# Optimization experiments

Measured on AMD Instinct MI355X. Metric: run time of the kernel, lower is better.

Reference implementation:

```python
import jax, jax.numpy as jnp
import numpy as np

D_K = 512  # attn_dim

def setup_inputs() -> dict:
    key = jax.random.key(0)
    ks = jax.random.split(key, 10)
    B, S, D, A, Dv = 8, 2048, 1024, 512, 512
    Q = jax.random.normal(ks[0], (B, S, D), dtype=jnp.float32)
    K = jax.random.normal(ks[1], (B, S, D), dtype=jnp.float32)
    V = jax.random.normal(ks[2], (B, S, D), dtype=jnp.float32)
    attn_mask = jax.random.randint(ks[3], (B, S, S), 0, 2, dtype=jnp.int32)
    s = 1.0 / np.sqrt(D)
    Wq = jax.random.normal(ks[4], (A, D), dtype=jnp.float32) * s
    bq = jnp.zeros((A,), dtype=jnp.float32)
    Wk = jax.random.normal(ks[5], (A, D), dtype=jnp.float32) * s
    bk = jnp.zeros((A,), dtype=jnp.float32)
    Wv = jax.random.normal(ks[6], (Dv, D), dtype=jnp.float32) * s
    bv = jnp.zeros((Dv,), dtype=jnp.float32)
    return {"Q": Q, "K": K, "V": V, "attn_mask": attn_mask,
            "Wq": Wq, "bq": bq, "Wk": Wk, "bk": bk, "Wv": Wv, "bv": bv}

def reference(Q, K, V, attn_mask, Wq, bq, Wk, bk, Wv, bv):
    # Linear projections (torch Linear: x @ W.T + b)
    Qp = jnp.einsum('bsd,ad->bsa', Q, Wq) + bq          # [B,S,A]
    Kp = jnp.einsum('bsd,ad->bsa', K, Wk) + bk          # [B,S,A]
    WV = jnp.einsum('bsd,vd->bsv', V, Wv) + bv          # [B,S,Dv]
    scale = 1.0 / np.sqrt(D_K).astype(np.float32)
    scores = jnp.einsum('bqa,bka->bqk', Qp, Kp) * scale  # [B,S,S]
    scores = scores + attn_mask.astype(scores.dtype) * (-1e9)
    scores = jnp.swapaxes(scores, -1, -2)               # transpose BEFORE softmax
    attn = jax.nn.softmax(scores, axis=-1)              # normalize over query axis
    selfOutput = jnp.einsum('bkq,bqv->bkv', attn, WV)   # [B,S,Dv]
    return selfOutput, attn
```

## Files before the change

### kernel.cpp

```cpp
#include <hip/hip_runtime.h>
#include <stdint.h>

#define B_N   8
#define S_N   2048
#define D_N   1024
#define A_N   512
#define DV_N  512

typedef __attribute__((ext_vector_type(8))) short bf16x8;
typedef __attribute__((ext_vector_type(4))) float f32x4;

__device__ __forceinline__ unsigned short f2bf(float x) {
    union { float f; unsigned int u; } v; v.f = x;
    return (unsigned short)((v.u + 0x7fffu + ((v.u >> 16) & 1u)) >> 16);
}
__device__ __forceinline__ float bf2f(unsigned short h) {
    union { unsigned int u; float f; } v; v.u = ((unsigned int)h) << 16;
    return v.f;
}

__global__ void cvt3_f32_bf16(const float* __restrict__ s0, const float* __restrict__ s1,
                              const float* __restrict__ s2,
                              unsigned short* __restrict__ d0, unsigned short* __restrict__ d1,
                              unsigned short* __restrict__ d2, int n4) {
    const float* s = (blockIdx.z == 0) ? s0 : (blockIdx.z == 1) ? s1 : s2;
    unsigned short* d = (blockIdx.z == 0) ? d0 : (blockIdx.z == 1) ? d1 : d2;
    int i = blockIdx.x * blockDim.x + threadIdx.x;
    if (i >= n4) return;
    float4 v = ((const float4*)s)[i];
    ushort4 o;
    o.x = f2bf(v.x); o.y = f2bf(v.y); o.z = f2bf(v.z); o.w = f2bf(v.w);
    ((ushort4*)d)[i] = o;
}

__global__ void zero_f32(float* __restrict__ p, int n) {
    int i = blockIdx.x * blockDim.x + threadIdx.x;
    if (i < n) p[i] = 0.0f;
}

__device__ __forceinline__ void gld_lds16(const void* g, void* l) {
    __builtin_amdgcn_global_load_lds(
        (const __attribute__((address_space(1))) unsigned int*)g,
        (__attribute__((address_space(3))) unsigned int*)l, 16, 0, 0);
}

__global__ __launch_bounds__(256) void pack_maskT(const int* __restrict__ mask,
                                                  unsigned int* __restrict__ mpT) {
    __shared__ int tile[64 * 129];
    const int b  = blockIdx.z;
    const int q0 = blockIdx.y * 64;
    const int k0 = blockIdx.x * 128;
    const int tid = threadIdx.x;
    const long long base = (long long)b * S_N * S_N;
#pragma unroll
    for (int it = 0; it < 8; ++it) {
        int c = it * 256 + tid;
        int row  = c >> 5;
        int col4 = (c & 31) * 4;
        int4 v = *(const int4*)&mask[base + (long long)(q0 + row) * S_N + k0 + col4];
        int* d = &tile[row * 129 + col4];
        d[0] = v.x; d[1] = v.y; d[2] = v.z; d[3] = v.w;
    }
    __syncthreads();
    const int wave = tid >> 6, lane = tid & 63;
#pragma unroll
    for (int kk = 0; kk < 32; ++kk) {
        const int k = wave * 32 + kk;
        const int v = tile[lane * 129 + k];
        const unsigned long long bal = __ballot(v != 0);
        if (lane == 0) {
            unsigned int* o = &mpT[(long long)(b * S_N + k0 + k) * 64 + (q0 >> 5)];
            o[0] = (unsigned int)bal;
            o[1] = (unsigned int)(bal >> 32);
        }
    }
}

template <int MODE>
__global__ __launch_bounds__(256) void gemm_nt(
    const unsigned short* __restrict__ A, const unsigned short* __restrict__ B,
    const unsigned short* __restrict__ B2,
    void* __restrict__ C, const float* __restrict__ bias, const float* __restrict__ bias2,
    const unsigned int* __restrict__ mpT, float* __restrict__ rowsum,
    int M, int N, int K,
    long long sA, long long sB, long long sC, float scale)
{
    __shared__ __align__(16) unsigned short As[128 * 32];
    __shared__ __align__(16) unsigned short Bs[128 * 32];

    const int tid  = threadIdx.x;
    const int wave = tid >> 6;
    const int lane = tid & 63;
    const int lrow = lane & 15;
    const int quad = lane >> 4;
    const int wm = wave & 1;
    const int wn = wave >> 1;
    const int b  = blockIdx.z;
    const int m0 = blockIdx.y * 128;
    const int n0 = blockIdx.x * 128;

    const unsigned short* Ab = A + (long long)b * sA;
    const unsigned short* Bsel = (MODE == 0 && blockIdx.y >= 128) ? B2 : B;
    const unsigned short* Bb = Bsel + (long long)b * sB;
    const float* bias_s = (MODE == 0 && blockIdx.y >= 128) ? bias2 : bias;

    f32x4 acc[4][4];
#pragma unroll
    for (int i = 0; i < 4; ++i)
#pragma unroll
        for (int j = 0; j < 4; ++j) acc[i][j] = (f32x4){0.f, 0.f, 0.f, 0.f};

    const int srow = lane >> 2;
    const int scol = (lane & 3) * 8;

    for (int kt = 0; kt < K; kt += 32) {
#pragma unroll
        for (int t = 0; t < 2; ++t) {
            const int seg = t * 4 + wave;
            const unsigned short* ga =
                Ab + (long long)(m0 + seg * 16 + srow) * K + kt + scol;
            gld_lds16(ga, &As[seg * 16 * 32]);
            const unsigned short* gb =
                Bb + (long long)(n0 + seg * 16 + srow) * K + kt + scol;
            gld_lds16(gb, &Bs[seg * 16 * 32]);
        }
        __syncthreads();

        bf16x8 af[4], bfr[4];
#pragma unroll
        for (int i = 0; i < 4; ++i)
            af[i] = *(const bf16x8*)&As[(wm * 64 + i * 16 + lrow) * 32 + quad * 8];
#pragma unroll
        for (int j = 0; j < 4; ++j)
            bfr[j] = *(const bf16x8*)&Bs[(wn * 64 + j * 16 + lrow) * 32 + quad * 8];
#pragma unroll
        for (int i = 0; i < 4; ++i)
#pragma unroll
            for (int j = 0; j < 4; ++j)
                acc[i][j] = __builtin_amdgcn_mfma_f32_16x16x32_bf16(
                    af[i], bfr[j], acc[i][j], 0, 0, 0);
        __syncthreads();
    }

    if (MODE == 0 || MODE == 1) {
#pragma unroll
        for (int i = 0; i < 4; ++i) {
            const int rowb = m0 + wm * 64 + i * 16 + quad * 4;
#pragma unroll
            for (int j = 0; j < 4; ++j) {
                const int col = n0 + wn * 64 + j * 16 + lrow;
#pragma unroll
                for (int r = 0; r < 4; ++r) {
                    const int row = rowb + r;
                    float v = acc[i][j][r];
                    v += (MODE == 0) ? bias_s[col] : bias_s[row];
                    (((unsigned short*)C) + (long long)b * sC)
                        [(long long)row * N + col] = f2bf(v);
                }
            }
        }
    } else if (MODE == 2) {
        unsigned short* Cb = ((unsigned short*)C) + (long long)b * sC;
        const unsigned int* mpb = mpT + ((long long)b * S_N) * 64;
        float* rs = rowsum + (long long)b * S_N;
#pragma unroll
        for (int i = 0; i < 4; ++i) {
#pragma unroll
            for (int r = 0; r < 4; ++r) {
                const int row = m0 + wm * 64 + i * 16 + quad * 4 + r;
                const unsigned int* mpr = mpb + (long long)row * 64;
                float rsum = 0.0f;
#pragma unroll
                for (int j = 0; j < 4; ++j) {
                    const int col = n0 + wn * 64 + j * 16 + lrow;
                    const float v = acc[i][j][r] * scale;
                    const unsigned int w = mpr[col >> 5];
                    const float e = ((w >> (col & 31)) & 1u) ? 0.0f : __expf(v);
                    const unsigned short h = f2bf(e);
                    Cb[(long long)row * S_N + col] = h;
                    rsum += bf2f(h);
                }
                rsum += __shfl_xor(rsum, 1);
                rsum += __shfl_xor(rsum, 2);
                rsum += __shfl_xor(rsum, 4);
                rsum += __shfl_xor(rsum, 8);
                if (lrow == 0) atomicAdd(&rs[row], rsum);
            }
        }
    } else {
        float* Cb = ((float*)C) + (long long)b * sC;
        const float* rs = rowsum + (long long)b * S_N;
#pragma unroll
        for (int i = 0; i < 4; ++i) {
#pragma unroll
            for (int r = 0; r < 4; ++r) {
                const int row = m0 + wm * 64 + i * 16 + quad * 4 + r;
                const float inv = 1.0f / rs[row];
#pragma unroll
                for (int j = 0; j < 4; ++j) {
                    const int col = n0 + wn * 64 + j * 16 + lrow;
                    Cb[(long long)row * N + col] = acc[i][j][r] * inv;
                }
            }
        }
    }
}

__global__ __launch_bounds__(256) void normalize_rows(
    const unsigned short* __restrict__ ebf, const float* __restrict__ rowsum,
    float* __restrict__ attn)
{
    const long long row = blockIdx.x;
    const float inv = 1.0f / rowsum[row];
    const ushort4* src = (const ushort4*)(ebf + row * S_N);
    float4* dst = (float4*)(attn + row * S_N);
    const int tid = threadIdx.x;
#pragma unroll
    for (int t = 0; t < 2; ++t) {
        ushort4 h = src[tid + t * 256];
        float4 o;
        o.x = bf2f(h.x) * inv;
        o.y = bf2f(h.y) * inv;
        o.z = bf2f(h.z) * inv;
        o.w = bf2f(h.w) * inv;
        dst[tid + t * 256] = o;
    }
}

extern "C" void kernel_launch(void* const* d_in, const int* in_sizes, int n_in,
                              void* d_out, int out_size, void* d_ws, size_t ws_size,
                              hipStream_t stream) {
    const float* Q    = (const float*)d_in[0];
    const float* K    = (const float*)d_in[1];
    const float* V    = (const float*)d_in[2];
    const int*   mask = (const int*)d_in[3];
    const float* Wq   = (const float*)d_in[4];
    const float* bq   = (const float*)d_in[5];
    const float* Wk   = (const float*)d_in[6];
    const float* bk   = (const float*)d_in[7];
    const float* Wv   = (const float*)d_in[8];
    const float* bv   = (const float*)d_in[9];

    float* out      = (float*)d_out;
    float* attn_out = out + (long long)B_N * S_N * DV_N;

    unsigned short* Qbf  = (unsigned short*)d_ws;
    unsigned short* Kbf  = Qbf + (long long)B_N * S_N * D_N;
    unsigned short* attn_bf = Qbf;
    unsigned short* Vbf  = Kbf + (long long)B_N * S_N * D_N;
    unsigned short* Wqbf = Vbf + (long long)B_N * S_N * D_N;
    unsigned short* Wkbf = Wqbf + (long long)A_N * D_N;
    unsigned short* Wvbf = Wkbf + (long long)A_N * D_N;
    unsigned short* Qp   = Wvbf + (long long)DV_N * D_N;
    unsigned short* Kp   = Qp + (long long)B_N * S_N * A_N;
    unsigned short* WVt  = Kp + (long long)B_N * S_N * A_N;
    unsigned int*   mpT  = (unsigned int*)(WVt + (long long)B_N * DV_N * S_N);
    float*          rowsum = (float*)(mpT + (long long)B_N * S_N * 64);

    const float scale = 0.044194173824159216f;

    zero_f32<<<dim3((B_N * S_N) / 256), dim3(256), 0, stream>>>(rowsum, B_N * S_N);
    pack_maskT<<<dim3(S_N / 128, S_N / 64, B_N), dim3(256), 0, stream>>>(mask, mpT);

    {
        int n4 = (int)((long long)B_N * S_N * D_N / 4);
        cvt3_f32_bf16<<<dim3((n4 + 255) / 256, 1, 3), dim3(256), 0, stream>>>(
            Q, K, V, Qbf, Kbf, Vbf, n4);
        int w4 = (int)((long long)A_N * D_N / 4);
        cvt3_f32_bf16<<<dim3((w4 + 255) / 256, 1, 3), dim3(256), 0, stream>>>(
            Wq, Wk, Wv, Wqbf, Wkbf, Wvbf, w4);
    }

    gemm_nt<0><<<dim3(A_N / 128, (2 * B_N * S_N) / 128, 1), dim3(256), 0, stream>>>(
        Qbf, Wqbf, Wkbf, (void*)Qp, bq, bk, nullptr, nullptr,
        2 * B_N * S_N, A_N, D_N, 0, 0, 0, 1.0f);
    gemm_nt<1><<<dim3(S_N / 128, DV_N / 128, B_N), dim3(256), 0, stream>>>(
        Wvbf, Vbf, nullptr, (void*)WVt, bv, nullptr, nullptr, nullptr,
        DV_N, S_N, D_N, 0, (long long)S_N * D_N, (long long)DV_N * S_N, 1.0f);
    gemm_nt<2><<<dim3(S_N / 128, S_N / 128, B_N), dim3(256), 0, stream>>>(
        Kp, Qp, nullptr, (void*)attn_bf, nullptr, nullptr, mpT, rowsum,
        S_N, S_N, A_N, (long long)S_N * A_N, (long long)S_N * A_N,
        (long long)S_N * S_N, scale);
    normalize_rows<<<dim3(B_N * S_N), dim3(256), 0, stream>>>(attn_bf, rowsum, attn_out);
    gemm_nt<3><<<dim3(DV_N / 128, S_N / 128, B_N), dim3(256), 0, stream>>>(
        attn_bf, WVt, nullptr, (void*)out, nullptr, nullptr, nullptr, rowsum,
        S_N, DV_N, S_N, (long long)S_N * S_N, (long long)DV_N * S_N,
        (long long)S_N * DV_N, 1.0f);
}
```

Baseline: 678.0 us.

## Add 256x256-tile 8-wave pipelined GEMM for projection and score kernels

Introduces gemm_nt8, a 512-thread kernel with 256x256 output tiles and a double-buffered 128KB LDS. Global-to-LDS loads are interleaved with MFMA phases under explicit vmcnt waits and setprio, and it replaces the 128x128 GEMM for the Q/K projection and the masked score/exp stage. The aim is more data reuse per tile and overlap of loads with matrix math. In exchange it raises register and LDS pressure, which cuts occupancy, and its hand-tuned waitcnt sequencing is fragile.

```diff
diff --git a/kernel.cpp b/kernel.cpp
--- a/kernel.cpp
+++ b/kernel.cpp
@@ -206,6 +206,171 @@
     }
 }
 
+#define VMCNT(n) asm volatile("s_waitcnt vmcnt(" #n ")" ::: "memory")
+
+template <int MODE>
+__global__ __launch_bounds__(512, 2) void gemm_nt8(
+    const unsigned short* __restrict__ A, const unsigned short* __restrict__ B,
+    const unsigned short* __restrict__ B2,
+    void* __restrict__ C, const float* __restrict__ bias, const float* __restrict__ bias2,
+    const unsigned int* __restrict__ mpT, float* __restrict__ rowsum,
+    int M, int N, int K,
+    long long sA, long long sB, long long sC, float scale)
+{
+    extern __shared__ unsigned short sm[];
+
+    const int tid  = threadIdx.x;
+    const int w    = tid >> 6;
+    const int lane = tid & 63;
+    const int lrow = lane & 15;
+    const int quad = lane >> 4;
+    const int wmSel = w >> 2;
+    const int wn    = w & 3;
+    const int bhSel = wn >> 1;
+    const int b  = blockIdx.z;
+    const int m0 = blockIdx.y * 256;
+    const int n0 = blockIdx.x * 256;
+
+    const unsigned short* Ab = A + (long long)b * sA;
+    const unsigned short* Bsel = (MODE == 0 && blockIdx.y >= 64) ? B2 : B;
+    const unsigned short* Bb = Bsel + (long long)b * sB;
+    const float* bias_s = (MODE == 0 && blockIdx.y >= 64) ? bias2 : bias;
+
+    const int csw0 = ((quad ^ (lrow & 7)) << 4);
+    const int csw1 = csw0 ^ 64;
+    const int cswSt = (((lane & 7) ^ (lane >> 3)) << 3);
+
+    const unsigned short* srcA =
+        Ab + (size_t)(m0 + (w >> 2) * 128 + (w & 3) * 16 + (lane >> 3)) * K + cswSt;
+    const unsigned short* srcB =
+        Bb + (size_t)(n0 + (w >> 2) * 128 + ((w >> 1) & 1) * 64 + (w & 1) * 16 + (lane >> 3)) * K + cswSt;
+
+#define STAGE_A(par, mq, tk) do {                                              \
+        const unsigned short* s_ = srcA + (size_t)(mq) * 64 * K + (size_t)(tk) * 64; \
+        unsigned short* d_ = &sm[(par) * 16384 + (w >> 2) * 8192 +             \
+                                 ((mq) * 64 + (w & 3) * 16) * 64];             \
+        gld_lds16(s_, d_);                                                     \
+        gld_lds16(s_ + 8 * (size_t)K, d_ + 8 * 64);                            \
+    } while (0)
+
+#define STAGE_B(par, nq, tk) do {                                              \
+        const unsigned short* s_ = srcB + (size_t)(nq) * 32 * K + (size_t)(tk) * 64; \
+        unsigned short* d_ = &sm[32768 + (par) * 16384 + (w >> 2) * 8192 +     \
+                                 (((w >> 1) & 1) * 64 + (nq) * 32 + (w & 1) * 16) * 64]; \
+        gld_lds16(s_, d_);                                                     \
+        gld_lds16(s_ + 8 * (size_t)K, d_ + 8 * 64);                            \
+    } while (0)
+
+    f32x4 acc[8][4];
+#pragma unroll
+    for (int i = 0; i < 8; ++i)
+#pragma unroll
+        for (int j = 0; j < 4; ++j) acc[i][j] = (f32x4){0.f, 0.f, 0.f, 0.f};
+
+#define PHASE(par, mq, nq, STAGE_STMT, WAIT_STMT) do {                         \
+        bf16x8 af[4][2], bfr[2][2];                                            \
+        const int abase_ = (par) * 16384 + wmSel * 8192 + (mq) * 4096;         \
+        _Pragma("unroll")                                                      \
+        for (int m_ = 0; m_ < 4; ++m_) {                                       \
+            af[m_][0] = *(const bf16x8*)&sm[abase_ + (m_ * 16 + lrow) * 64 + (csw0 >> 1)]; \
+            af[m_][1] = *(const bf16x8*)&sm[abase_ + (m_ * 16 + lrow) * 64 + (csw1 >> 1)]; \
+        }                                                                      \
+        const int bbase_ = 32768 + (par) * 16384 + bhSel * 8192 +              \
+                           ((wn & 1) * 64 + (nq) * 32) * 64;                   \
+        _Pragma("unroll")                                                      \
+        for (int n_ = 0; n_ < 2; ++n_) {                                       \
+            bfr[n_][0] = *(const bf16x8*)&sm[bbase_ + (n_ * 16 + lrow) * 64 + (csw0 >> 1)]; \
+            bfr[n_][1] = *(const bf16x8*)&sm[bbase_ + (n_ * 16 + lrow) * 64 + (csw1 >> 1)]; \
+        }                                                                      \
+        STAGE_STMT;                                                            \
+        WAIT_STMT;                                                             \
+        __builtin_amdgcn_s_barrier();                                          \
+        __builtin_amdgcn_s_setprio(1);                                         \
+        _Pragma("unroll")                                                      \
+        for (int m_ = 0; m_ < 4; ++m_)                                         \
+            _Pragma("unroll")                                                  \
+            for (int n_ = 0; n_ < 2; ++n_) {                                   \
+                acc[(mq)*4+m_][(nq)*2+n_] = __builtin_amdgcn_mfma_f32_16x16x32_bf16( \
+                    af[m_][0], bfr[n_][0], acc[(mq)*4+m_][(nq)*2+n_], 0, 0, 0); \
+                acc[(mq)*4+m_][(nq)*2+n_] = __builtin_amdgcn_mfma_f32_16x16x32_bf16( \
+                    af[m_][1], bfr[n_][1], acc[(mq)*4+m_][(nq)*2+n_], 0, 0, 0); \
+            }                                                                  \
+        __builtin_amdgcn_s_setprio(0);                                         \
+        __builtin_amdgcn_s_barrier();                                          \
+    } while (0)
+
+    const int NT = K >> 6;
+
+    STAGE_A(0, 0, 0); STAGE_B(0, 0, 0);
+    STAGE_A(0, 1, 0); STAGE_B(0, 1, 0);
+    STAGE_A(1, 0, 1); STAGE_B(1, 0, 1);
+    VMCNT(8);
+    __builtin_amdgcn_s_barrier();
+
+    for (int t = 0; t < NT; t += 2) {
+        const int t2 = (t + 2 < NT) ? t + 2 : NT - 1;
+        const int t3 = (t + 3 < NT) ? t + 3 : NT - 1;
+        PHASE(0, 0, 0, STAGE_A(1, 1, t + 1), VMCNT(6));
+        PHASE(0, 0, 1, STAGE_B(1, 1, t + 1), VMCNT(10));
+        PHASE(0, 1, 0, STAGE_A(0, 0, t2),    (void)0);
+        PHASE(0, 1, 1, STAGE_B(0, 0, t2),    VMCNT(8));
+        PHASE(1, 0, 0, STAGE_A(0, 1, t2),    VMCNT(6));
+        PHASE(1, 0, 1, STAGE_B(0, 1, t2),    VMCNT(10));
+        PHASE(1, 1, 0, STAGE_A(1, 0, t3),    (void)0);
+        PHASE(1, 1, 1, STAGE_B(1, 0, t3),    VMCNT(8));
+    }
+    VMCNT(0);
+
+    if (MODE == 0) {
+#pragma unroll
+        for (int i = 0; i < 8; ++i) {
+            const int rowb = m0 + wmSel * 128 + i * 16 + quad * 4;
+#pragma unroll
+            for (int j = 0; j < 4; ++j) {
+                const int col = n0 + wn * 64 + j * 16 + lrow;
+#pragma unroll
+                for (int r = 0; r < 4; ++r) {
+                    const int row = rowb + r;
+                    float v = acc[i][j][r] + bias_s[col];
+                    (((unsigned short*)C) + (long long)b * sC)
+                        [(long long)row * N + col] = f2bf(v);
+                }
+            }
+        }
+    } else {
+        unsigned short* Cb = ((unsigned short*)C) + (long long)b * sC;
+        const unsigned int* mpb = mpT + ((long long)b * S_N) * 64;
+        float* rs = rowsum + (long long)b * S_N;
+#pragma unroll
+        for (int i = 0; i < 8; ++i) {
+#pragma unroll
+            for (int r = 0; r < 4; ++r) {
+                const int row = m0 + wmSel * 128 + i * 16 + quad * 4 + r;
+                const unsigned int* mpr = mpb + (long long)row * 64;
+                float rsum = 0.0f;
+#pragma unroll
+                for (int j = 0; j < 4; ++j) {
+                    const int col = n0 + wn * 64 + j * 16 + lrow;
+                    const float v = acc[i][j][r] * scale;
+                    const unsigned int wbits = mpr[col >> 5];
+                    const float e = ((wbits >> (col & 31)) & 1u) ? 0.0f : __expf(v);
+                    const unsigned short h = f2bf(e);
+                    Cb[(long long)row * S_N + col] = h;
+                    rsum += bf2f(h);
+                }
+                rsum += __shfl_xor(rsum, 1);
+                rsum += __shfl_xor(rsum, 2);
+                rsum += __shfl_xor(rsum, 4);
+                rsum += __shfl_xor(rsum, 8);
+                if (lrow == 0) atomicAdd(&rs[row], rsum);
+            }
+        }
+    }
+#undef PHASE
+#undef STAGE_A
+#undef STAGE_B
+}
+
 __global__ __launch_bounds__(256) void normalize_rows(
     const unsigned short* __restrict__ ebf, const float* __restrict__ rowsum,
     float* __restrict__ attn)
@@ -259,6 +424,15 @@
 
     const float scale = 0.044194173824159216f;
 
+    static bool attrSet = false;
+    if (!attrSet) {
+        hipFuncSetAttribute(reinterpret_cast<const void*>(&gemm_nt8<0>),
+                            hipFuncAttributeMaxDynamicSharedMemorySize, 131072);
+        hipFuncSetAttribute(reinterpret_cast<const void*>(&gemm_nt8<2>),
+                            hipFuncAttributeMaxDynamicSharedMemorySize, 131072);
+        attrSet = true;
+    }
+
     zero_f32<<<dim3((B_N * S_N) / 256), dim3(256), 0, stream>>>(rowsum, B_N * S_N);
     pack_maskT<<<dim3(S_N / 128, S_N / 64, B_N), dim3(256), 0, stream>>>(mask, mpT);
 
@@ -271,13 +445,13 @@
             Wq, Wk, Wv, Wqbf, Wkbf, Wvbf, w4);
     }
 
-    gemm_nt<0><<<dim3(A_N / 128, (2 * B_N * S_N) / 128, 1), dim3(256), 0, stream>>>(
+    gemm_nt8<0><<<dim3(A_N / 256, (2 * B_N * S_N) / 256, 1), dim3(512), 131072, stream>>>(
         Qbf, Wqbf, Wkbf, (void*)Qp, bq, bk, nullptr, nullptr,
         2 * B_N * S_N, A_N, D_N, 0, 0, 0, 1.0f);
     gemm_nt<1><<<dim3(S_N / 128, DV_N / 128, B_N), dim3(256), 0, stream>>>(
         Wvbf, Vbf, nullptr, (void*)WVt, bv, nullptr, nullptr, nullptr,
         DV_N, S_N, D_N, 0, (long long)S_N * D_N, (long long)DV_N * S_N, 1.0f);
-    gemm_nt<2><<<dim3(S_N / 128, S_N / 128, B_N), dim3(256), 0, stream>>>(
+    gemm_nt8<2><<<dim3(S_N / 256, S_N / 256, B_N), dim3(512), 131072, stream>>>(
         Kp, Qp, nullptr, (void*)attn_bf, nullptr, nullptr, mpT, rowsum,
         S_N, S_N, A_N, (long long)S_N * A_N, (long long)S_N * A_N,
         (long long)S_N * S_N, scale);
```

New measurement: 644.2 us. -5.0%, faster.
